# Kernel optimization log

Hardware: AMD Instinct MI355X
Metric: run time of the kernel (lower is better)

The kernel has to match this reference:

```python
import jax, jax.numpy as jnp
import numpy as np

MOVING_RATE = 0.999

def _l2norm(x, eps=1e-12):
    # matches F.normalize(dim=-1): x / max(||x||, eps)
    return x / jnp.maximum(jnp.linalg.norm(x, axis=-1, keepdims=True), eps)

def setup_inputs() -> dict:
    k = jax.random.key(0)
    k1, k2, k3 = jax.random.split(k, 3)
    B, S, K, D = 8192, 14, 512, 256
    return {
        "key": jax.random.normal(k1, (B, S, D), dtype=jnp.float32),
        "value": jax.random.normal(k2, (B, S, D), dtype=jnp.float32),
        "memory": jax.random.normal(k3, (S, K, D), dtype=jnp.float32),
    }

def reference(key, value, memory):
    # key, value: (B, S, D); memory: (S, K, D). update=True path, all slots batched.
    K = memory.shape[1]
    xn = _l2norm(key)                                   # (B,S,D)
    mn = _l2norm(memory)                                # (S,K,D)
    score = jnp.einsum('bsd,skd->bsk', xn, mn)          # (B,S,K)

    # --- EMA codebook update (value is detached in the original) ---
    v = jax.lax.stop_gradient(value)
    ind = jnp.argmax(score, axis=-1)                    # (B,S)
    oh = jax.nn.one_hot(ind, K, dtype=value.dtype)      # (B,S,K)
    oh_sum = oh.sum(axis=0)                             # (S,K)
    emb_sum = jnp.einsum('bsd,bsk->skd', v, oh)         # (S,K,D)
    emb_mean = emb_sum / (oh_sum[..., None] + 1e-6)
    new_mem = memory * MOVING_RATE + emb_mean * (1.0 - MOVING_RATE)

    # --- re-score against updated codebook ---
    score2 = jnp.einsum('bsd,skd->bsk', xn, _l2norm(new_mem))
    ind2 = jnp.argmax(score2, axis=-1)
    oh2 = jax.nn.one_hot(ind2, K, dtype=value.dtype)    # (B,S,K)

    # note: original adds value[:, 0, :] (slot 0) for EVERY slot i — kept faithfully
    out = value[:, :1, :] + jnp.einsum('bsk,skd->bsd', oh2, new_mem)  # (B,S,D)
    return out, new_mem
```

## Files before the change

### kernel.cpp

```cpp
#include <hip/hip_runtime.h>
#include <cstddef>
#include <cstdint>

#define B_ 8192
#define S_ 14
#define K_ 512
#define D_ 256

#define CERT_C 6.0e-5f

typedef __attribute__((ext_vector_type(8))) short bfx8;
typedef __attribute__((ext_vector_type(4))) float fx4;

typedef __attribute__((address_space(3))) unsigned int       lds_u32;
typedef const __attribute__((address_space(1))) unsigned int glb_u32;

__device__ __forceinline__ void gload16(const void* g, void* l) {
    __builtin_amdgcn_global_load_lds((glb_u32*)g, (lds_u32*)l, 16, 0, 0);
}

__device__ __forceinline__ unsigned short f2bf(float x) {
    union { float f; unsigned int u; } v; v.f = x;
    unsigned int r = (v.u + 0x7FFFu + ((v.u >> 16) & 1u)) >> 16;
    return (unsigned short)r;
}
__device__ __forceinline__ float bf2f(unsigned short h) {
    union { unsigned int u; float f; } v; v.u = ((unsigned int)h) << 16;
    return v.f;
}

__global__ __launch_bounds__(64) void rownorm_kernel(
    const float* __restrict__ rows, float* __restrict__ invn)
{
    const int row  = blockIdx.x;
    const int lane = threadIdx.x;
    const float4 v = *reinterpret_cast<const float4*>(rows + (size_t)row * D_ + lane * 4);
    float ss = v.x * v.x + v.y * v.y + v.z * v.z + v.w * v.w;
    #pragma unroll
    for (int m = 32; m >= 1; m >>= 1) ss += __shfl_xor(ss, m, 64);
    if (lane == 0) invn[row] = 1.0f / fmaxf(sqrtf(ss), 1e-12f);
}

__global__ __launch_bounds__(256) void split_key2_kernel(
    const float* __restrict__ key,
    unsigned short* __restrict__ ph, unsigned short* __restrict__ pm,
    float* __restrict__ keynorm)
{
    const int w    = threadIdx.x >> 6;
    const int lane = threadIdx.x & 63;
    const int b    = blockIdx.x * 4 + w;
    const int s    = blockIdx.y;
    const float4 x = *reinterpret_cast<const float4*>(
        key + ((size_t)b * S_ + s) * D_ + lane * 4);
    const size_t o = ((size_t)s * B_ + b) * D_ + lane * 4;

    float xs[4] = { x.x, x.y, x.z, x.w };
    unsigned short hh[4], mm[4];
    #pragma unroll
    for (int i = 0; i < 4; ++i) {
        unsigned short a = f2bf(xs[i]);
        float r1 = xs[i] - bf2f(a);
        hh[i] = a; mm[i] = f2bf(r1);
    }
    *reinterpret_cast<ushort4*>(ph + o) = make_ushort4(hh[0], hh[1], hh[2], hh[3]);
    *reinterpret_cast<ushort4*>(pm + o) = make_ushort4(mm[0], mm[1], mm[2], mm[3]);

    float ss = x.x * x.x + x.y * x.y + x.z * x.z + x.w * x.w;
    #pragma unroll
    for (int m = 32; m >= 1; m >>= 1) ss += __shfl_xor(ss, m, 64);
    if (lane == 0) keynorm[(size_t)s * B_ + b] = sqrtf(ss);
}

__global__ __launch_bounds__(64) void splitnorm_mem2_kernel(
    const float* __restrict__ mem,
    unsigned short* __restrict__ ph, unsigned short* __restrict__ pm,
    float* __restrict__ invn)
{
    const int row  = blockIdx.x;
    const int lane = threadIdx.x;
    const size_t e = (size_t)row * D_ + lane * 4;
    const float4 x = *reinterpret_cast<const float4*>(mem + e);

    float xs[4] = { x.x, x.y, x.z, x.w };
    unsigned short hh[4], mm[4];
    #pragma unroll
    for (int i = 0; i < 4; ++i) {
        unsigned short a = f2bf(xs[i]);
        float r1 = xs[i] - bf2f(a);
        hh[i] = a; mm[i] = f2bf(r1);
    }
    *reinterpret_cast<ushort4*>(ph + e) = make_ushort4(hh[0], hh[1], hh[2], hh[3]);
    *reinterpret_cast<ushort4*>(pm + e) = make_ushort4(mm[0], mm[1], mm[2], mm[3]);

    float ss = x.x * x.x + x.y * x.y + x.z * x.z + x.w * x.w;
    #pragma unroll
    for (int m = 32; m >= 1; m >>= 1) ss += __shfl_xor(ss, m, 64);
    if (lane == 0) invn[row] = 1.0f / fmaxf(sqrtf(ss), 1e-12f);
}

__global__ __launch_bounds__(256, 3) void gemm_argmax3_kernel(
    const unsigned short* __restrict__ kh, const unsigned short* __restrict__ km,
    const unsigned short* __restrict__ mh, const unsigned short* __restrict__ mm_,
    const float* __restrict__ invn,
    float* __restrict__ pV1, int* __restrict__ pI1, float* __restrict__ pV2)
{
    __shared__ short T[4][128 * 32];
    __shared__ float sInv[128];
    __shared__ float bV1[128][2];
    __shared__ int   bI1[128][2];
    __shared__ float bV2[128][2];

    const int orig = blockIdx.x;
    const int wg   = (orig & 7) * 448 + (orig >> 3);
    const int by   = wg & 3;
    const int bx   = (wg >> 2) & 63;
    const int s    = wg >> 8;

    const int t    = threadIdx.x;
    const int b0   = bx * 128;
    const int n0   = by * 128;
    const int w    = t >> 6;
    const int lane = t & 63;
    const int wm   = w >> 1, wn = w & 1;
    const int lr   = lane & 15, lg = lane >> 4;

    const size_t sB = (size_t)s * B_;
    const size_t sK = (size_t)s * K_;

    const unsigned short* __restrict__ APl[2] = { kh, km };
    const unsigned short* __restrict__ BPl[2] = { mh, mm_ };

    fx4 acc[4][4];
    #pragma unroll
    for (int i = 0; i < 4; ++i)
        #pragma unroll
        for (int j = 0; j < 4; ++j) acc[i][j] = (fx4)0.0f;

    const int rsub = lane >> 2;
    const int csw  = (((lane & 3) ^ ((lane >> 3) & 3)) * 8);
    const int rdof = ((lg ^ ((lr >> 1) & 3)) * 8);

    for (int dc = 0; dc < 8; ++dc) {
        const int dco = dc * 32 + csw;
        #pragma unroll
        for (int p = 0; p < 2; ++p) {
            #pragma unroll
            for (int u = 0; u < 2; ++u) {
                const int R0 = w * 32 + u * 16;
                gload16(APl[p] + (sB + b0 + R0 + rsub) * D_ + dco, &T[p][R0 * 32]);
                gload16(BPl[p] + (sK + n0 + R0 + rsub) * D_ + dco, &T[2 + p][R0 * 32]);
            }
        }
        __syncthreads();

        bfx8 bf[2][4];
        #pragma unroll
        for (int bp = 0; bp < 2; ++bp)
            #pragma unroll
            for (int j = 0; j < 4; ++j)
                bf[bp][j] = *reinterpret_cast<const bfx8*>(
                    &T[2 + bp][(wn * 64 + j * 16 + lr) * 32 + rdof]);

        #pragma unroll
        for (int ap = 0; ap < 2; ++ap) {
            bfx8 af[4];
            #pragma unroll
            for (int i = 0; i < 4; ++i)
                af[i] = *reinterpret_cast<const bfx8*>(
                    &T[ap][(wm * 64 + i * 16 + lr) * 32 + rdof]);
            #pragma unroll
            for (int bp = 0; bp < 2 - ap; ++bp) {
                __builtin_amdgcn_s_setprio(1);
                #pragma unroll
                for (int i = 0; i < 4; ++i)
                    #pragma unroll
                    for (int j = 0; j < 4; ++j)
                        acc[i][j] = __builtin_amdgcn_mfma_f32_16x16x32_bf16(
                            af[i], bf[bp][j], acc[i][j], 0, 0, 0);
                __builtin_amdgcn_s_setprio(0);
            }
        }
        __syncthreads();
    }

    if (t < 128) sInv[t] = invn[sK + n0 + t];
    __syncthreads();

    #pragma unroll
    for (int i = 0; i < 4; ++i) {
        #pragma unroll
        for (int r = 0; r < 4; ++r) {
            float v1 = -3.4e38f, v2 = -3.4e38f; int i1 = 0x7fffffff;
            #pragma unroll
            for (int j = 0; j < 4; ++j) {
                const int kloc = wn * 64 + j * 16 + lr;
                const float v  = acc[i][j][r] * sInv[kloc];
                const int  kg  = n0 + kloc;
                if (v > v1 || (v == v1 && kg < i1)) { v2 = v1; v1 = v; i1 = kg; }
                else if (v > v2) v2 = v;
            }
            #pragma unroll
            for (int msk = 1; msk < 16; msk <<= 1) {
                const float ov1 = __shfl_xor(v1, msk, 64);
                const int   oi1 = __shfl_xor(i1, msk, 64);
                const float ov2 = __shfl_xor(v2, msk, 64);
                const bool op = (ov1 > v1) || (ov1 == v1 && oi1 < i1);
                if (op) { v2 = fmaxf(v1, ov2); v1 = ov1; i1 = oi1; }
                else    { v2 = fmaxf(ov1, v2); }
            }
            if (lr == 0) {
                const int mrow = wm * 64 + i * 16 + lg * 4 + r;
                bV1[mrow][wn] = v1; bI1[mrow][wn] = i1; bV2[mrow][wn] = v2;
            }
        }
    }
    __syncthreads();

    if (t < 128) {
        float v1 = bV1[t][0]; int i1 = bI1[t][0]; float v2 = bV2[t][0];
        const float ov1 = bV1[t][1]; const int oi1 = bI1[t][1]; const float ov2 = bV2[t][1];
        const bool op = (ov1 > v1) || (ov1 == v1 && oi1 < i1);
        if (op) { v2 = fmaxf(v1, ov2); v1 = ov1; i1 = oi1; }
        else    { v2 = fmaxf(ov1, v2); }
        const size_t o = ((size_t)s * 4 + by) * B_ + b0 + t;
        pV1[o] = v1; pI1[o] = i1; pV2[o] = v2;
    }
}

__global__ __launch_bounds__(256) void combine_cert_kernel(
    const float* __restrict__ pV1, const int* __restrict__ pI1,
    const float* __restrict__ pV2, const float* __restrict__ keynorm,
    int* __restrict__ ind, int* __restrict__ ambCnt, int* __restrict__ ambList)
{
    const int idx = blockIdx.x * 256 + threadIdx.x;
    const int s   = idx >> 13;
    const int b   = idx & 8191;
    float V1 = -3.4e38f, V2 = -3.4e38f; int I1 = 0x7fffffff;
    #pragma unroll
    for (int nb = 0; nb < 4; ++nb) {
        const size_t o = ((size_t)s * 4 + nb) * B_ + b;
        const float v1 = pV1[o]; const int i1 = pI1[o]; const float v2 = pV2[o];
        const bool op = (v1 > V1) || (v1 == V1 && i1 < I1);
        if (op) { V2 = fmaxf(V1, v2); V1 = v1; I1 = i1; }
        else    { V2 = fmaxf(v1, V2); }
    }
    ind[idx] = I1;
    const float eps = CERT_C * keynorm[idx];
    if (V1 - V2 < 2.0f * eps) {
        const int p = atomicAdd(ambCnt, 1);
        ambList[p] = idx;
    }
}

__global__ __launch_bounds__(64) void zero2_kernel(
    int* __restrict__ c1, int* __restrict__ c2)
{
    if (threadIdx.x == 0) { *c1 = 0; *c2 = 0; }
}

__global__ __launch_bounds__(256) void rescore_kernel(
    const int* __restrict__ ambCnt, const int* __restrict__ ambList,
    const float* __restrict__ key, const float* __restrict__ mem,
    const float* __restrict__ invn, int* __restrict__ ind)
{
    __shared__ double sV[4];
    __shared__ int    sI[4];
    const int n    = *ambCnt;
    const int t    = threadIdx.x;
    const int w    = t >> 6;
    const int lane = t & 63;
    for (int li = blockIdx.x; li < n; li += gridDim.x) {
        const int row = ambList[li];
        const int s = row >> 13, b = row & 8191;
        const float4 kv = *reinterpret_cast<const float4*>(
            key + ((size_t)b * S_ + s) * D_ + lane * 4);
        const double k0 = kv.x, k1 = kv.y, k2 = kv.z, k3 = kv.w;
        const float* __restrict__ mbase = mem + (size_t)s * K_ * D_;
        const float* __restrict__ ibase = invn + (size_t)s * K_;

        double bv = -1.0e300; int bk = 0x7fffffff;
        for (int kq = 0; kq < 128; kq += 4) {
            double d[4];
            #pragma unroll
            for (int u = 0; u < 4; ++u) {
                const int k = w * 128 + kq + u;
                const float4 mv = *reinterpret_cast<const float4*>(
                    mbase + (size_t)k * D_ + lane * 4);
                d[u] = k0 * mv.x + k1 * mv.y + k2 * mv.z + k3 * mv.w;
            }
            #pragma unroll
            for (int m = 32; m >= 1; m >>= 1)
                #pragma unroll
                for (int u = 0; u < 4; ++u) d[u] += __shfl_xor(d[u], m, 64);
            #pragma unroll
            for (int u = 0; u < 4; ++u) {
                const int k = w * 128 + kq + u;
                const double sc = d[u] * (double)ibase[k];
                if (sc > bv || (sc == bv && k < bk)) { bv = sc; bk = k; }
            }
        }
        if (lane == 0) { sV[w] = bv; sI[w] = bk; }
        __syncthreads();
        if (t == 0) {
            double v = sV[0]; int bi = sI[0];
            #pragma unroll
            for (int g = 1; g < 4; ++g)
                if (sV[g] > v || (sV[g] == v && sI[g] < bi)) { v = sV[g]; bi = sI[g]; }
            ind[row] = bi;
        }
        __syncthreads();
    }
}

__global__ __launch_bounds__(256) void gather_out_kernel(
    const int* __restrict__ ind2, const float* __restrict__ value,
    const float* __restrict__ newmem, float* __restrict__ out)
{
    const int row  = blockIdx.x * 4 + (threadIdx.x >> 6);
    const int lane = threadIdx.x & 63;
    const int s    = row >> 13;
    const int b    = row & 8191;
    const int bi   = ind2[row];
    const float4 vv = *reinterpret_cast<const float4*>(
        value + (size_t)b * (S_ * D_) + lane * 4);
    const float4 mmv = *reinterpret_cast<const float4*>(
        newmem + ((size_t)s * K_ + bi) * D_ + lane * 4);
    float4 o4;
    o4.x = vv.x + mmv.x; o4.y = vv.y + mmv.y;
    o4.z = vv.z + mmv.z; o4.w = vv.w + mmv.w;
    *reinterpret_cast<float4*>(out + ((size_t)b * S_ + s) * D_ + lane * 4) = o4;
}

__global__ __launch_bounds__(256) void u1_hist_kernel(
    const int* __restrict__ ind1, int* __restrict__ hist)
{
    __shared__ int h[K_];
    const int t = threadIdx.x, c = blockIdx.x, s = blockIdx.y;
    h[t] = 0; h[t + 256] = 0;
    __syncthreads();
    const int k = ind1[(size_t)s * B_ + c * 256 + t];
    atomicAdd(&h[k], 1);
    __syncthreads();
    hist[((size_t)s * 32 + c) * K_ + t]       = h[t];
    hist[((size_t)s * 32 + c) * K_ + t + 256] = h[t + 256];
}

__global__ __launch_bounds__(512) void u2_scan_kernel(
    int* __restrict__ hist, int* __restrict__ cnt, int* __restrict__ offs)
{
    __shared__ int sc[K_];
    const int k = threadIdx.x, s = blockIdx.x;
    int run = 0;
    for (int c = 0; c < 32; ++c) {
        const size_t o = ((size_t)s * 32 + c) * K_ + k;
        const int x = hist[o];
        hist[o] = run;
        run += x;
    }
    cnt[s * K_ + k] = run;
    sc[k] = run;
    __syncthreads();
    for (int off = 1; off < K_; off <<= 1) {
        int v = (k >= off) ? sc[k - off] : 0;
        __syncthreads();
        sc[k] += v;
        __syncthreads();
    }
    offs[s * K_ + k] = sc[k] - run;
}

__global__ __launch_bounds__(256) void u3_scatter_kernel(
    const int* __restrict__ ind1, const int* __restrict__ hist,
    const int* __restrict__ offs, int* __restrict__ csr)
{
    __shared__ int sk[256];
    const int t = threadIdx.x, c = blockIdx.x, s = blockIdx.y;
    const int b = c * 256 + t;
    const int k = ind1[(size_t)s * B_ + b];
    sk[t] = k;
    __syncthreads();
    int rank = 0;
    for (int j = 0; j < t; ++j) rank += (sk[j] == k);
    const int pos = offs[s * K_ + k] + hist[((size_t)s * 32 + c) * K_ + k] + rank;
    csr[(size_t)s * B_ + pos] = b;
}

__global__ __launch_bounds__(64) void u4_gather_kernel(
    const int* __restrict__ csr, const int* __restrict__ cnt,
    const int* __restrict__ offs, const float* __restrict__ value,
    const float* __restrict__ memory, float* __restrict__ newmem)
{
    const int k = blockIdx.x, s = blockIdx.y, lane = threadIdx.x;
    const int n = cnt[s * K_ + k];
    const int base = offs[s * K_ + k];
    float4 a; a.x = a.y = a.z = a.w = 0.0f;
    for (int i = 0; i < n; ++i) {
        const int b = csr[(size_t)s * B_ + base + i];
        const float4 v = *reinterpret_cast<const float4*>(
            value + ((size_t)b * S_ + s) * D_ + lane * 4);
        a.x += v.x; a.y += v.y; a.z += v.z; a.w += v.w;
    }
    const float inv = 1.0f / ((float)n + 1e-6f);
    const size_t o = ((size_t)s * K_ + k) * D_ + lane * 4;
    const float4 mo = *reinterpret_cast<const float4*>(memory + o);
    float4 r;
    r.x = mo.x * 0.999f + a.x * inv * 0.001f;
    r.y = mo.y * 0.999f + a.y * inv * 0.001f;
    r.z = mo.z * 0.999f + a.z * inv * 0.001f;
    r.w = mo.w * 0.999f + a.w * inv * 0.001f;
    *reinterpret_cast<float4*>(newmem + o) = r;
}

template <int MODE>
__global__ __launch_bounds__(256) void score_argmax_kernel(
    const float* __restrict__ key, const float* __restrict__ mem,
    const float* __restrict__ invn, const float* __restrict__ value,
    float* __restrict__ out, int* __restrict__ ind_out)
{
    __shared__ __align__(16) float kt[64][36];
    __shared__ __align__(16) float mt[64][36];
    __shared__ float redV[64][16];
    __shared__ int   redI[64][16];

    const int t  = threadIdx.x;
    const int s  = blockIdx.y;
    const int b0 = blockIdx.x * 64;
    const int tb = t & 15;
    const int tk = t >> 4;

    float best[4]; int bidx[4];
    #pragma unroll
    for (int i = 0; i < 4; ++i) { best[i] = -3.4e38f; bidx[i] = 0; }

    for (int kc = 0; kc < 8; ++kc) {
        float acc[4][4];
        #pragma unroll
        for (int i = 0; i < 4; ++i)
            #pragma unroll
            for (int j = 0; j < 4; ++j) acc[i][j] = 0.0f;

        for (int dc = 0; dc < 8; ++dc) {
            #pragma unroll
            for (int u = 0; u < 2; ++u) {
                const int f = t + u * 256;
                const int row = f >> 3;
                const int c4 = f & 7;
                *reinterpret_cast<float4*>(&kt[row][c4 * 4]) =
                    *reinterpret_cast<const float4*>(
                        key + (((size_t)(b0 + row)) * S_ + s) * D_ + dc * 32 + c4 * 4);
                *reinterpret_cast<float4*>(&mt[row][c4 * 4]) =
                    *reinterpret_cast<const float4*>(
                        mem + (((size_t)s * K_) + kc * 64 + row) * D_ + dc * 32 + c4 * 4);
            }
            __syncthreads();
            #pragma unroll
            for (int d4 = 0; d4 < 8; ++d4) {
                float4 a[4], b[4];
                #pragma unroll
                for (int i = 0; i < 4; ++i)
                    a[i] = *reinterpret_cast<const float4*>(&kt[tb + i * 16][d4 * 4]);
                #pragma unroll
                for (int j = 0; j < 4; ++j)
                    b[j] = *reinterpret_cast<const float4*>(&mt[tk + j * 16][d4 * 4]);
                #pragma unroll
                for (int i = 0; i < 4; ++i)
                    #pragma unroll
                    for (int j = 0; j < 4; ++j)
                        acc[i][j] += a[i].x * b[j].x + a[i].y * b[j].y +
                                     a[i].z * b[j].z + a[i].w * b[j].w;
            }
            __syncthreads();
        }
        #pragma unroll
        for (int j = 0; j < 4; ++j) {
            const int kabs = kc * 64 + tk + j * 16;
            const float inv = invn[s * K_ + kabs];
            #pragma unroll
            for (int i = 0; i < 4; ++i) {
                const float v = acc[i][j] * inv;
                if (v > best[i] || (v == best[i] && kabs < bidx[i])) {
                    best[i] = v; bidx[i] = kabs;
                }
            }
        }
    }
    #pragma unroll
    for (int i = 0; i < 4; ++i) {
        redV[tb + i * 16][tk] = best[i];
        redI[tb + i * 16][tk] = bidx[i];
    }
    __syncthreads();
    if (t < 64) {
        float bv = redV[t][0]; int bi = redI[t][0];
        #pragma unroll
        for (int g = 1; g < 16; ++g) {
            const float v = redV[t][g]; const int ix = redI[t][g];
            if (v > bv || (v == bv && ix < bi)) { bv = v; bi = ix; }
        }
        if (MODE == 0) ind_out[(size_t)s * B_ + b0 + t] = bi;
        else           redI[t][0] = bi;
    }
    if (MODE == 1) {
        __syncthreads();
        const int w = t >> 6, lane = t & 63;
        for (int r = w; r < 64; r += 4) {
            const int bg = b0 + r;
            const int kk = redI[r][0];
            const float4 vv = *reinterpret_cast<const float4*>(
                value + (size_t)bg * (S_ * D_) + lane * 4);
            const float4 mmv = *reinterpret_cast<const float4*>(
                mem + ((size_t)s * K_ + kk) * D_ + lane * 4);
            float4 o;
            o.x = vv.x + mmv.x; o.y = vv.y + mmv.y;
            o.z = vv.z + mmv.z; o.w = vv.w + mmv.w;
            *reinterpret_cast<float4*>(
                out + (((size_t)bg) * S_ + s) * D_ + lane * 4) = o;
        }
    }
}

__global__ __launch_bounds__(256) void update_kernel(
    const int* __restrict__ ind1, const float* __restrict__ value,
    const float* __restrict__ memory, float* __restrict__ newmem)
{
    const int k0 = blockIdx.x * 4, s = blockIdx.y, t = threadIdx.x;
    __shared__ int sIdx[256];
    float a0 = 0.f, a1 = 0.f, a2 = 0.f, a3 = 0.f;
    int c0 = 0, c1 = 0, c2 = 0, c3 = 0;
    for (int b0 = 0; b0 < B_; b0 += 256) {
        sIdx[t] = ind1[(size_t)s * B_ + b0 + t];
        __syncthreads();
        for (int bb = 0; bb < 256; ++bb) {
            const int ix = sIdx[bb];
            const unsigned r = (unsigned)(ix - k0);
            if (r < 4u) {
                const float v = value[(((size_t)(b0 + bb)) * S_ + s) * D_ + t];
                if      (r == 0u) { a0 += v; ++c0; }
                else if (r == 1u) { a1 += v; ++c1; }
                else if (r == 2u) { a2 += v; ++c2; }
                else              { a3 += v; ++c3; }
            }
        }
        __syncthreads();
    }
    const float accs[4] = { a0, a1, a2, a3 };
    const int   cns [4] = { c0, c1, c2, c3 };
    #pragma unroll
    for (int kk = 0; kk < 4; ++kk) {
        const size_t off = ((size_t)s * K_ + k0 + kk) * D_ + t;
        const float mean = accs[kk] / ((float)cns[kk] + 1e-6f);
        newmem[off] = memory[off] * 0.999f + mean * 0.001f;
    }
}

extern "C" void kernel_launch(void* const* d_in, const int* in_sizes, int n_in,
                              void* d_out, int out_size, void* d_ws, size_t ws_size,
                              hipStream_t stream)
{
    const float* key    = (const float*)d_in[0];
    const float* value  = (const float*)d_in[1];
    const float* memory = (const float*)d_in[2];

    float* out    = (float*)d_out;
    float* newmem = out + (size_t)B_ * S_ * D_;

    const size_t keyPlane = (size_t)S_ * B_ * D_;
    const size_t memPlane = (size_t)S_ * K_ * D_;
    char* p = (char*)d_ws;
    size_t need = 0;
    auto alloc = [&](size_t bytes) -> char* {
        char* r = p + need;
        need += (bytes + 255) & ~(size_t)255;
        return r;
    };
    unsigned short* kh   = (unsigned short*)alloc(keyPlane * 2);
    unsigned short* km   = (unsigned short*)alloc(keyPlane * 2);
    unsigned short* mh   = (unsigned short*)alloc(memPlane * 2);
    unsigned short* mm   = (unsigned short*)alloc(memPlane * 2);
    float* invn    = (float*)alloc((size_t)S_ * K_ * 4);
    float* keynorm = (float*)alloc((size_t)S_ * B_ * 4);
    float* pV1     = (float*)alloc((size_t)S_ * 4 * B_ * 4);
    int*   pI1     = (int*)  alloc((size_t)S_ * 4 * B_ * 4);
    float* pV2     = (float*)alloc((size_t)S_ * 4 * B_ * 4);
    int*   ind1    = (int*)  alloc((size_t)S_ * B_ * 4);
    int*   ind2    = (int*)  alloc((size_t)S_ * B_ * 4);
    int*   amb1Cnt = (int*)  alloc(256);
    int*   amb2Cnt = (int*)  alloc(256);
    int*   amb1Lst = (int*)  alloc((size_t)S_ * B_ * 4);
    int*   amb2Lst = (int*)  alloc((size_t)S_ * B_ * 4);
    int*   hist    = (int*)  alloc((size_t)S_ * 32 * K_ * 4);
    int*   cnt     = (int*)  alloc((size_t)S_ * K_ * 4);
    int*   offs    = (int*)  alloc((size_t)S_ * K_ * 4);
    int*   csr     = (int*)  alloc((size_t)S_ * B_ * 4);

    if (ws_size >= need) {
        split_key2_kernel<<<dim3(B_ / 4, S_), 256, 0, stream>>>(key, kh, km, keynorm);
        splitnorm_mem2_kernel<<<dim3(S_ * K_), 64, 0, stream>>>(memory, mh, mm, invn);
        zero2_kernel<<<dim3(1), 64, 0, stream>>>(amb1Cnt, amb2Cnt);

        gemm_argmax3_kernel<<<dim3(3584), 256, 0, stream>>>(
            kh, km, mh, mm, invn, pV1, pI1, pV2);
        combine_cert_kernel<<<dim3((S_ * B_) / 256), 256, 0, stream>>>(
            pV1, pI1, pV2, keynorm, ind1, amb1Cnt, amb1Lst);
        rescore_kernel<<<dim3(1024), 256, 0, stream>>>(
            amb1Cnt, amb1Lst, key, memory, invn, ind1);

        u1_hist_kernel<<<dim3(32, S_), 256, 0, stream>>>(ind1, hist);
        u2_scan_kernel<<<dim3(S_), 512, 0, stream>>>(hist, cnt, offs);
        u3_scatter_kernel<<<dim3(32, S_), 256, 0, stream>>>(ind1, hist, offs, csr);
        u4_gather_kernel<<<dim3(K_, S_), 64, 0, stream>>>(csr, cnt, offs, value, memory, newmem);

        splitnorm_mem2_kernel<<<dim3(S_ * K_), 64, 0, stream>>>(newmem, mh, mm, invn);

        gemm_argmax3_kernel<<<dim3(3584), 256, 0, stream>>>(
            kh, km, mh, mm, invn, pV1, pI1, pV2);
        combine_cert_kernel<<<dim3((S_ * B_) / 256), 256, 0, stream>>>(
            pV1, pI1, pV2, keynorm, ind2, amb2Cnt, amb2Lst);
        rescore_kernel<<<dim3(1024), 256, 0, stream>>>(
            amb2Cnt, amb2Lst, key, newmem, invn, ind2);

        gather_out_kernel<<<dim3((S_ * B_) / 4), 256, 0, stream>>>(
            ind2, value, newmem, out);
    } else {
        float* invn1 = (float*)d_ws;
        float* invn2 = invn1 + S_ * K_;
        int*   find1 = (int*)(invn2 + S_ * K_);

        rownorm_kernel<<<dim3(S_ * K_), 64, 0, stream>>>(memory, invn1);
        score_argmax_kernel<0><<<dim3(B_ / 64, S_), 256, 0, stream>>>(
            key, memory, invn1, nullptr, nullptr, find1);
        update_kernel<<<dim3(K_ / 4, S_), 256, 0, stream>>>(find1, value, memory, newmem);
        rownorm_kernel<<<dim3(S_ * K_), 64, 0, stream>>>(newmem, invn2);
        score_argmax_kernel<1><<<dim3(B_ / 64, S_), 256, 0, stream>>>(
            key, newmem, invn2, value, out, nullptr);
    }
}
```

Before: 507.2 us.

## Track top-3 scores to rescore ambiguous rows against only two candidates

The GEMM argmax epilogue now keeps the top two indices and the third-best value instead of only the top one and the second-best value. Rows whose top two scores are within the certification margin but clearly separated from the third are sent to a cheap pair rescore that computes two fp64 dot products. Only rows where the third candidate is also close fall back to the full 512-way fp64 rescore. This removes most of the full-codebook rescoring work, at the cost of extra shuffles, LDS traffic and two more partial-result arrays written in the GEMM epilogue.

```diff
diff --git a/kernel.cpp b/kernel.cpp
--- a/kernel.cpp
+++ b/kernel.cpp
@@ -27,6 +27,18 @@
 __device__ __forceinline__ float bf2f(unsigned short h) {
     union { unsigned int u; float f; } v; v.u = ((unsigned int)h) << 16;
     return v.f;
+}
+
+__device__ __forceinline__ void top3_ins(
+    float v, int k, float& v1, int& i1, float& v2, int& i2, float& v3)
+{
+    if (v > v1 || (v == v1 && k < i1)) {
+        v3 = v2; v2 = v1; i2 = i1; v1 = v; i1 = k;
+    } else if (v > v2 || (v == v2 && k < i2)) {
+        v3 = v2; v2 = v; i2 = k;
+    } else if (v > v3) {
+        v3 = v;
+    }
 }
 
 __global__ __launch_bounds__(64) void rownorm_kernel(
@@ -102,13 +114,16 @@
     const unsigned short* __restrict__ kh, const unsigned short* __restrict__ km,
     const unsigned short* __restrict__ mh, const unsigned short* __restrict__ mm_,
     const float* __restrict__ invn,
-    float* __restrict__ pV1, int* __restrict__ pI1, float* __restrict__ pV2)
+    float* __restrict__ pV1, int* __restrict__ pI1,
+    float* __restrict__ pV2, int* __restrict__ pI2, float* __restrict__ pV3)
 {
     __shared__ short T[4][128 * 32];
     __shared__ float sInv[128];
     __shared__ float bV1[128][2];
     __shared__ int   bI1[128][2];
     __shared__ float bV2[128][2];
+    __shared__ int   bI2[128][2];
+    __shared__ float bV3[128][2];
 
     const int orig = blockIdx.x;
     const int wg   = (orig & 7) * 448 + (orig >> 3);
@@ -190,87 +205,137 @@
     for (int i = 0; i < 4; ++i) {
         #pragma unroll
         for (int r = 0; r < 4; ++r) {
-            float v1 = -3.4e38f, v2 = -3.4e38f; int i1 = 0x7fffffff;
+            float v1 = -3.4e38f, v2 = -3.4e38f, v3 = -3.4e38f;
+            int i1 = 0x7fffffff, i2 = 0x7fffffff;
             #pragma unroll
             for (int j = 0; j < 4; ++j) {
                 const int kloc = wn * 64 + j * 16 + lr;
                 const float v  = acc[i][j][r] * sInv[kloc];
-                const int  kg  = n0 + kloc;
-                if (v > v1 || (v == v1 && kg < i1)) { v2 = v1; v1 = v; i1 = kg; }
-                else if (v > v2) v2 = v;
+                top3_ins(v, n0 + kloc, v1, i1, v2, i2, v3);
             }
             #pragma unroll
             for (int msk = 1; msk < 16; msk <<= 1) {
                 const float ov1 = __shfl_xor(v1, msk, 64);
                 const int   oi1 = __shfl_xor(i1, msk, 64);
                 const float ov2 = __shfl_xor(v2, msk, 64);
-                const bool op = (ov1 > v1) || (ov1 == v1 && oi1 < i1);
-                if (op) { v2 = fmaxf(v1, ov2); v1 = ov1; i1 = oi1; }
-                else    { v2 = fmaxf(ov1, v2); }
+                const int   oi2 = __shfl_xor(i2, msk, 64);
+                const float ov3 = __shfl_xor(v3, msk, 64);
+                top3_ins(ov1, oi1, v1, i1, v2, i2, v3);
+                top3_ins(ov2, oi2, v1, i1, v2, i2, v3);
+                v3 = fmaxf(v3, ov3);
             }
             if (lr == 0) {
                 const int mrow = wm * 64 + i * 16 + lg * 4 + r;
-                bV1[mrow][wn] = v1; bI1[mrow][wn] = i1; bV2[mrow][wn] = v2;
+                bV1[mrow][wn] = v1; bI1[mrow][wn] = i1;
+                bV2[mrow][wn] = v2; bI2[mrow][wn] = i2;
+                bV3[mrow][wn] = v3;
             }
         }
     }
     __syncthreads();
 
     if (t < 128) {
-        float v1 = bV1[t][0]; int i1 = bI1[t][0]; float v2 = bV2[t][0];
-        const float ov1 = bV1[t][1]; const int oi1 = bI1[t][1]; const float ov2 = bV2[t][1];
-        const bool op = (ov1 > v1) || (ov1 == v1 && oi1 < i1);
-        if (op) { v2 = fmaxf(v1, ov2); v1 = ov1; i1 = oi1; }
-        else    { v2 = fmaxf(ov1, v2); }
+        float v1 = bV1[t][0], v2 = bV2[t][0], v3 = bV3[t][0];
+        int   i1 = bI1[t][0], i2 = bI2[t][0];
+        top3_ins(bV1[t][1], bI1[t][1], v1, i1, v2, i2, v3);
+        top3_ins(bV2[t][1], bI2[t][1], v1, i1, v2, i2, v3);
+        v3 = fmaxf(v3, bV3[t][1]);
         const size_t o = ((size_t)s * 4 + by) * B_ + b0 + t;
-        pV1[o] = v1; pI1[o] = i1; pV2[o] = v2;
-    }
-}
-
-__global__ __launch_bounds__(256) void combine_cert_kernel(
+        pV1[o] = v1; pI1[o] = i1; pV2[o] = v2; pI2[o] = i2; pV3[o] = v3;
+    }
+}
+
+__global__ __launch_bounds__(256) void combine_cert3_kernel(
     const float* __restrict__ pV1, const int* __restrict__ pI1,
-    const float* __restrict__ pV2, const float* __restrict__ keynorm,
-    int* __restrict__ ind, int* __restrict__ ambCnt, int* __restrict__ ambList)
+    const float* __restrict__ pV2, const int* __restrict__ pI2,
+    const float* __restrict__ pV3, const float* __restrict__ keynorm,
+    int* __restrict__ ind, int* __restrict__ cand2,
+    int* __restrict__ pairCnt, int* __restrict__ pairList,
+    int* __restrict__ fullCnt, int* __restrict__ fullList)
 {
     const int idx = blockIdx.x * 256 + threadIdx.x;
     const int s   = idx >> 13;
     const int b   = idx & 8191;
-    float V1 = -3.4e38f, V2 = -3.4e38f; int I1 = 0x7fffffff;
+    float V1 = -3.4e38f, V2 = -3.4e38f, V3 = -3.4e38f;
+    int I1 = 0x7fffffff, I2 = 0x7fffffff;
     #pragma unroll
     for (int nb = 0; nb < 4; ++nb) {
         const size_t o = ((size_t)s * 4 + nb) * B_ + b;
-        const float v1 = pV1[o]; const int i1 = pI1[o]; const float v2 = pV2[o];
-        const bool op = (v1 > V1) || (v1 == V1 && i1 < I1);
-        if (op) { V2 = fmaxf(V1, v2); V1 = v1; I1 = i1; }
-        else    { V2 = fmaxf(v1, V2); }
+        top3_ins(pV1[o], pI1[o], V1, I1, V2, I2, V3);
+        top3_ins(pV2[o], pI2[o], V1, I1, V2, I2, V3);
+        V3 = fmaxf(V3, pV3[o]);
     }
     ind[idx] = I1;
-    const float eps = CERT_C * keynorm[idx];
-    if (V1 - V2 < 2.0f * eps) {
-        const int p = atomicAdd(ambCnt, 1);
-        ambList[p] = idx;
-    }
-}
-
-__global__ __launch_bounds__(64) void zero2_kernel(
-    int* __restrict__ c1, int* __restrict__ c2)
-{
-    if (threadIdx.x == 0) { *c1 = 0; *c2 = 0; }
-}
-
-__global__ __launch_bounds__(256) void rescore_kernel(
-    const int* __restrict__ ambCnt, const int* __restrict__ ambList,
+    const float eps2 = 2.0f * CERT_C * keynorm[idx];
+    if (V1 - V2 < eps2) {
+        if (V1 - V3 > eps2) {
+            cand2[idx] = I2;
+            const int p = atomicAdd(pairCnt, 1);
+            pairList[p] = idx;
+        } else {
+            const int p = atomicAdd(fullCnt, 1);
+            fullList[p] = idx;
+        }
+    }
+}
+
+__global__ __launch_bounds__(64) void zero4_kernel(
+    int* __restrict__ c1, int* __restrict__ c2,
+    int* __restrict__ c3, int* __restrict__ c4)
+{
+    if (threadIdx.x == 0) { *c1 = 0; *c2 = 0; *c3 = 0; *c4 = 0; }
+}
+
+__global__ __launch_bounds__(256) void rescore_pair_kernel(
+    const int* __restrict__ pairCnt, const int* __restrict__ pairList,
+    const float* __restrict__ key, const float* __restrict__ mem,
+    const float* __restrict__ invn, const int* __restrict__ cand2,
+    int* __restrict__ ind)
+{
+    const int n    = *pairCnt;
+    const int w    = threadIdx.x >> 6;
+    const int lane = threadIdx.x & 63;
+    for (int li = blockIdx.x * 4 + w; li < n; li += gridDim.x * 4) {
+        const int row = pairList[li];
+        const int s = row >> 13, b = row & 8191;
+        const int i1 = ind[row], i2 = cand2[row];
+        const float4 kv = *reinterpret_cast<const float4*>(
+            key + ((size_t)b * S_ + s) * D_ + lane * 4);
+        const float4 m1 = *reinterpret_cast<const float4*>(
+            mem + ((size_t)s * K_ + i1) * D_ + lane * 4);
+        const float4 m2 = *reinterpret_cast<const float4*>(
+            mem + ((size_t)s * K_ + i2) * D_ + lane * 4);
+        double d1 = (double)kv.x * m1.x + (double)kv.y * m1.y
+                  + (double)kv.z * m1.z + (double)kv.w * m1.w;
+        double d2 = (double)kv.x * m2.x + (double)kv.y * m2.y
+                  + (double)kv.z * m2.z + (double)kv.w * m2.w;
+        #pragma unroll
+        for (int m = 32; m >= 1; m >>= 1) {
+            d1 += __shfl_xor(d1, m, 64);
+            d2 += __shfl_xor(d2, m, 64);
+        }
+        if (lane == 0) {
+            const double sc1 = d1 * (double)invn[(size_t)s * K_ + i1];
+            const double sc2 = d2 * (double)invn[(size_t)s * K_ + i2];
+            const bool take2 = (sc2 > sc1) || (sc2 == sc1 && i2 < i1);
+            if (take2) ind[row] = i2;
+        }
+    }
+}
+
+__global__ __launch_bounds__(256) void rescore_full_kernel(
+    const int* __restrict__ fullCnt, const int* __restrict__ fullList,
     const float* __restrict__ key, const float* __restrict__ mem,
     const float* __restrict__ invn, int* __restrict__ ind)
 {
     __shared__ double sV[4];
     __shared__ int    sI[4];
-    const int n    = *ambCnt;
+    const int n    = *fullCnt;
     const int t    = threadIdx.x;
     const int w    = t >> 6;
     const int lane = t & 63;
     for (int li = blockIdx.x; li < n; li += gridDim.x) {
-        const int row = ambList[li];
+        const int row = fullList[li];
         const int s = row >> 13, b = row & 8191;
         const float4 kv = *reinterpret_cast<const float4*>(
             key + ((size_t)b * S_ + s) * D_ + lane * 4);
@@ -582,12 +647,19 @@
     float* pV1     = (float*)alloc((size_t)S_ * 4 * B_ * 4);
     int*   pI1     = (int*)  alloc((size_t)S_ * 4 * B_ * 4);
     float* pV2     = (float*)alloc((size_t)S_ * 4 * B_ * 4);
+    int*   pI2     = (int*)  alloc((size_t)S_ * 4 * B_ * 4);
+    float* pV3     = (float*)alloc((size_t)S_ * 4 * B_ * 4);
     int*   ind1    = (int*)  alloc((size_t)S_ * B_ * 4);
     int*   ind2    = (int*)  alloc((size_t)S_ * B_ * 4);
-    int*   amb1Cnt = (int*)  alloc(256);
-    int*   amb2Cnt = (int*)  alloc(256);
-    int*   amb1Lst = (int*)  alloc((size_t)S_ * B_ * 4);
-    int*   amb2Lst = (int*)  alloc((size_t)S_ * B_ * 4);
+    int*   cand2   = (int*)  alloc((size_t)S_ * B_ * 4);
+    int*   pr1Cnt  = (int*)  alloc(256);
+    int*   fu1Cnt  = (int*)  alloc(256);
+    int*   pr2Cnt  = (int*)  alloc(256);
+    int*   fu2Cnt  = (int*)  alloc(256);
+    int*   pr1Lst  = (int*)  alloc((size_t)S_ * B_ * 4);
+    int*   fu1Lst  = (int*)  alloc((size_t)S_ * B_ * 4);
+    int*   pr2Lst  = (int*)  alloc((size_t)S_ * B_ * 4);
+    int*   fu2Lst  = (int*)  alloc((size_t)S_ * B_ * 4);
     int*   hist    = (int*)  alloc((size_t)S_ * 32 * K_ * 4);
     int*   cnt     = (int*)  alloc((size_t)S_ * K_ * 4);
     int*   offs    = (int*)  alloc((size_t)S_ * K_ * 4);
@@ -596,14 +668,17 @@
     if (ws_size >= need) {
         split_key2_kernel<<<dim3(B_ / 4, S_), 256, 0, stream>>>(key, kh, km, keynorm);
         splitnorm_mem2_kernel<<<dim3(S_ * K_), 64, 0, stream>>>(memory, mh, mm, invn);
-        zero2_kernel<<<dim3(1), 64, 0, stream>>>(amb1Cnt, amb2Cnt);
+        zero4_kernel<<<dim3(1), 64, 0, stream>>>(pr1Cnt, fu1Cnt, pr2Cnt, fu2Cnt);
 
         gemm_argmax3_kernel<<<dim3(3584), 256, 0, stream>>>(
-            kh, km, mh, mm, invn, pV1, pI1, pV2);
-        combine_cert_kernel<<<dim3((S_ * B_) / 256), 256, 0, stream>>>(
-            pV1, pI1, pV2, keynorm, ind1, amb1Cnt, amb1Lst);
-        rescore_kernel<<<dim3(1024), 256, 0, stream>>>(
-            amb1Cnt, amb1Lst, key, memory, invn, ind1);
+            kh, km, mh, mm, invn, pV1, pI1, pV2, pI2, pV3);
+        combine_cert3_kernel<<<dim3((S_ * B_) / 256), 256, 0, stream>>>(
+            pV1, pI1, pV2, pI2, pV3, keynorm, ind1, cand2,
+            pr1Cnt, pr1Lst, fu1Cnt, fu1Lst);
+        rescore_pair_kernel<<<dim3(1024), 256, 0, stream>>>(
+            pr1Cnt, pr1Lst, key, memory, invn, cand2, ind1);
+        rescore_full_kernel<<<dim3(512), 256, 0, stream>>>(
+            fu1Cnt, fu1Lst, key, memory, invn, ind1);
 
         u1_hist_kernel<<<dim3(32, S_), 256, 0, stream>>>(ind1, hist);
         u2_scan_kernel<<<dim3(S_), 512, 0, stream>>>(hist, cnt, offs);
@@ -613,11 +688,14 @@
         splitnorm_mem2_kernel<<<dim3(S_ * K_), 64, 0, stream>>>(newmem, mh, mm, invn);
 
         gemm_argmax3_kernel<<<dim3(3584), 256, 0, stream>>>(
-            kh, km, mh, mm, invn, pV1, pI1, pV2);
-        combine_cert_kernel<<<dim3((S_ * B_) / 256), 256, 0, stream>>>(
-            pV1, pI1, pV2, keynorm, ind2, amb2Cnt, amb2Lst);
-        rescore_kernel<<<dim3(1024), 256, 0, stream>>>(
-            amb2Cnt, amb2Lst, key, newmem, invn, ind2);
+            kh, km, mh, mm, invn, pV1, pI1, pV2, pI2, pV3);
+        combine_cert3_kernel<<<dim3((S_ * B_) / 256), 256, 0, stream>>>(
+            pV1, pI1, pV2, pI2, pV3, keynorm, ind2, cand2,
+            pr2Cnt, pr2Lst, fu2Cnt, fu2Lst);
+        rescore_pair_kernel<<<dim3(1024), 256, 0, stream>>>(
+            pr2Cnt, pr2Lst, key, newmem, invn, cand2, ind2);
+        rescore_full_kernel<<<dim3(512), 256, 0, stream>>>(
+            fu2Cnt, fu2Lst, key, newmem, invn, ind2);
 
         gather_out_kernel<<<dim3((S_ * B_) / 4), 256, 0, stream>>>(
             ind2, value, newmem, out);
```

Measured after the change: 607.6 us. 1.2x slower.
